# Performance work log

Hardware: AMD Instinct MI355X
Metric: run time of the kernel (lower is better)

Reference implementation:

```python
import jax, jax.numpy as jnp
import numpy as np

SCALE = 2
K = 8


def setup_inputs() -> dict:
    key = jax.random.key(0)
    k1, k2, k3 = jax.random.split(key, 3)
    m, f = 8192, 512
    y_patch = jax.random.normal(k1, (m, 64), dtype=jnp.float32)
    yd_patch = jax.random.normal(k2, (m, f), dtype=jnp.float32)
    idx_k = jax.random.randint(k3, (1, m, K), 0, m, dtype=jnp.int64)
    return {"y_patch": y_patch, "yd_patch": yd_patch, "idx_k": idx_k}


def reference(y_patch, yd_patch, idx_k):
    # y_patch: (m, f_q) -- only its leading dim m is used
    # yd_patch: (m, f) database features; idx_k: (1, m, k) neighbor indices into m
    m = y_patch.shape[0]
    yd = yd_patch.reshape(m, -1)          # (m=n, f)
    f = yd.shape[1]
    k = idx_k.shape[2]
    # Gather: torch builds z of shape (1, m, f, k) with z[0,q,c,j] = yd[idx_k[0,q,j], c].
    # Equivalent direct gather without materializing the expanded (1,m,f,n) tensor:
    z = yd[idx_k[0]]                      # (m, k, f)
    # torch permute(0,3,2,1): (1, m, f, k) -> (1, k, f, m)
    z = jnp.transpose(z, (1, 2, 0))       # (k, f, m)
    # view(1, k, f//scale, scale, m) then view(1, k*(f//scale), m*scale):
    # contiguous row-major, so a single reshape is exact.
    z_sr = z.reshape(1, k * (f // SCALE), m * SCALE)
    return z_sr
```

## Files before the change

### kernel.cpp

```cpp
#include <hip/hip_runtime.h>


#define QTILE 16
#define THREADS 256

__global__ __launch_bounds__(THREADS) void gather_transpose_kernel(
    const float* __restrict__ yd, const int* __restrict__ idx,
    float* __restrict__ out, int m, int f, int k)
{
    const int qbase = blockIdx.x * QTILE;
    const int j = blockIdx.y;
    const int t = threadIdx.x;
    const int ldst = f + 1;

    __shared__ int rows[QTILE];
    extern __shared__ float lds[];

    if (t < QTILE) rows[t] = idx[(size_t)(qbase + t) * k + j];
    __syncthreads();

    const int f4 = f >> 2;
    const int nvec = QTILE * f4;
    for (int lid = t; lid < nvec; lid += THREADS) {
        const int row = lid / f4;
        const int c4 = lid - row * f4;
        const float4 v = *reinterpret_cast<const float4*>(
            yd + (size_t)rows[row] * f + (c4 << 2));
        float* d = lds + row * ldst + (c4 << 2);
        d[0] = v.x; d[1] = v.y; d[2] = v.z; d[3] = v.w;
    }
    __syncthreads();

    const size_t out_j = (size_t)j * f * m;
    const int ntot = QTILE * f;
    for (int oid = t; oid < ntot; oid += THREADS) {
        const int q = oid & (QTILE - 1);
        const int c = oid >> 4;
        out[out_j + (size_t)c * m + qbase + q] = lds[q * ldst + c];
    }
}

extern "C" void kernel_launch(void* const* d_in, const int* in_sizes, int n_in,
                              void* d_out, int out_size, void* d_ws, size_t ws_size,
                              hipStream_t stream) {
    const float* yd = (const float*)d_in[1];
    const int* idx = (const int*)d_in[2];
    float* out = (float*)d_out;

    const int m = in_sizes[0] / 64;
    const int f = in_sizes[1] / m;
    const int k = in_sizes[2] / m;

    dim3 grid(m / QTILE, k);
    const size_t lds_bytes = (size_t)QTILE * (f + 1) * sizeof(float);
    hipLaunchKernelGGL(gather_transpose_kernel, grid, dim3(THREADS), lds_bytes,
                       stream, yd, idx, out, m, f, k);
}
```

Baseline: 165.3 us.

## Retile gather-transpose to 256-query by 32-feature blocks for long coalesced stores

Changes the block tile from 16 queries by all features to 256 queries by 32 features, with a 3D grid over query tiles, feature tiles and neighbors. Each thread now writes one query column across 32 feature rows, so stores form 1KB contiguous runs instead of 64-byte segments. The trade-off is that gather reads shrink to 128-byte chunks per indexed row, and the index loads are repeated per feature tile. It also switches to static shared memory.

After: 162.8 us. About the same (-1.5%).

```diff
diff --git a/kernel.cpp b/kernel.cpp
--- a/kernel.cpp
+++ b/kernel.cpp
@@ -1,42 +1,39 @@
 #include <hip/hip_runtime.h>
 
 
-#define QTILE 16
+#define Q 256
+#define C 32
 #define THREADS 256
 
 __global__ __launch_bounds__(THREADS) void gather_transpose_kernel(
     const float* __restrict__ yd, const int* __restrict__ idx,
     float* __restrict__ out, int m, int f, int k)
 {
-    const int qbase = blockIdx.x * QTILE;
-    const int j = blockIdx.y;
-    const int t = threadIdx.x;
-    const int ldst = f + 1;
+    const int qb = blockIdx.x * Q;
+    const int cb = blockIdx.y * C;
+    const int j  = blockIdx.z;
+    const int t  = threadIdx.x;
 
-    __shared__ int rows[QTILE];
-    extern __shared__ float lds[];
+    __shared__ int rows[Q];
+    __shared__ float lds[Q][C + 1];
 
-    if (t < QTILE) rows[t] = idx[(size_t)(qbase + t) * k + j];
+    rows[t] = idx[(size_t)(qb + t) * k + j];
     __syncthreads();
 
-    const int f4 = f >> 2;
-    const int nvec = QTILE * f4;
-    for (int lid = t; lid < nvec; lid += THREADS) {
-        const int row = lid / f4;
-        const int c4 = lid - row * f4;
+    for (int lid = t; lid < Q * (C / 4); lid += THREADS) {
+        const int row = lid >> 3;
+        const int ch  = lid & 7;
         const float4 v = *reinterpret_cast<const float4*>(
-            yd + (size_t)rows[row] * f + (c4 << 2));
-        float* d = lds + row * ldst + (c4 << 2);
+            yd + (size_t)rows[row] * f + cb + (ch << 2));
+        float* d = &lds[row][ch << 2];
         d[0] = v.x; d[1] = v.y; d[2] = v.z; d[3] = v.w;
     }
     __syncthreads();
 
-    const size_t out_j = (size_t)j * f * m;
-    const int ntot = QTILE * f;
-    for (int oid = t; oid < ntot; oid += THREADS) {
-        const int q = oid & (QTILE - 1);
-        const int c = oid >> 4;
-        out[out_j + (size_t)c * m + qbase + q] = lds[q * ldst + c];
+    float* p = out + (size_t)j * f * m + (size_t)cb * m + qb + t;
+    #pragma unroll 8
+    for (int c = 0; c < C; ++c) {
+        p[(size_t)c * m] = lds[t][c];
     }
 }
 
@@ -51,8 +48,7 @@
     const int f = in_sizes[1] / m;
     const int k = in_sizes[2] / m;
 
-    dim3 grid(m / QTILE, k);
-    const size_t lds_bytes = (size_t)QTILE * (f + 1) * sizeof(float);
-    hipLaunchKernelGGL(gather_transpose_kernel, grid, dim3(THREADS), lds_bytes,
+    dim3 grid(m / Q, f / C, k);
+    hipLaunchKernelGGL(gather_transpose_kernel, grid, dim3(THREADS), 0,
                        stream, yd, idx, out, m, f, k);
 }
```
